# Optimization experiments

Measured on AMD Instinct MI355X. Metric: run time of the kernel, lower is better.

Reference implementation:

```python
import jax, jax.numpy as jnp
import numpy as np

N, H, V, MAX_STEPS = 256, 128, 64, 4

def setup_inputs() -> dict:
    key = jax.random.key(0)
    ks = jax.random.split(key, 16)
    def w(k, shape, fan_in):
        return jax.random.normal(k, shape, dtype=jnp.float32) / np.sqrt(fan_in)
    inp = {}
    inp['node_embeddings'] = jax.random.normal(ks[0], (N, H), dtype=jnp.float32)
    inp['skip_embeddings'] = jax.random.normal(ks[1], (N, N, H), dtype=jnp.float32)
    inp['Wx'] = w(ks[2], (H, 4 * H), H)
    inp['Wh'] = w(ks[3], (H, 4 * H), H)
    inp['b'] = jnp.zeros((4 * H,), jnp.float32)
    inp['Wxs'] = w(ks[4], (H, 4 * H), H)
    inp['Whs'] = w(ks[5], (H, 4 * H), H)
    inp['bs'] = jnp.zeros((4 * H,), jnp.float32)
    inp['Wb'] = w(ks[6], (2 * H, 2), 2 * H)
    inp['bb'] = jnp.zeros((2,), jnp.float32)
    inp['Wk'] = w(ks[7], (H, H), H)
    inp['bk'] = jnp.zeros((H,), jnp.float32)
    inp['Wq'] = w(ks[8], (2 * H, H), 2 * H)
    inp['bq'] = jnp.zeros((H,), jnp.float32)
    inp['Wl'] = w(ks[9], (2 * H, 1), 2 * H)
    inp['bl'] = jnp.zeros((1,), jnp.float32)
    inp['Wd'] = w(ks[10], (2 * H, V), 2 * H)
    inp['bd'] = jnp.zeros((V,), jnp.float32)
    # valid skips only forward in the program (include diagonal = no-skip)
    inp['skip_mask'] = jnp.triu(jnp.ones((N, N), dtype=bool))
    inp['true_indexes'] = jax.random.randint(ks[11], (N,), 0, N, dtype=jnp.int32)
    inp['false_indexes'] = jax.random.randint(ks[12], (N,), 0, N, dtype=jnp.int32)
    inp['exit_index'] = N - 1
    return inp

def _lstm(c, h, x, Wx, Wh, b):
    gates = x @ Wx + h @ Wh + b  # [..., 4H]
    i, f, g, o = jnp.split(gates, 4, axis=-1)
    c2 = jax.nn.sigmoid(f) * c + jax.nn.sigmoid(i) * jnp.tanh(g)
    h2 = jax.nn.sigmoid(o) * jnp.tanh(c2)
    return c2, h2

def reference(node_embeddings, skip_embeddings, Wx, Wh, b, Wxs, Whs, bs,
              Wb, bb, Wk, bk, Wq, bq, Wl, bl, Wd, bd,
              skip_mask, true_indexes, false_indexes, exit_index):
    n, hdim = node_embeddings.shape
    eye = jnp.eye(n, dtype=node_embeddings.dtype)
    ip0 = jnp.zeros((n,), node_embeddings.dtype).at[0].set(1.0)
    c0 = jnp.zeros((n, hdim), node_embeddings.dtype)
    h0 = jnp.zeros((n, hdim), node_embeddings.dtype)
    keys = skip_embeddings @ Wk + bk  # [N,N,H] (input-only, precompute)

    def step(carry, _):
        ip, c, h = carry
        # per-node LSTM proposals
        c_p, h_p = _lstm(c, h, node_embeddings, Wx, Wh, b)  # [N,H]
        hid = jnp.concatenate([c_p, h_p], axis=-1)  # [N,2H]
        # skip proposals: carry of source i applied to skip embedding (i,j)
        c_sk, h_sk = _lstm(c[:, None, :], h[:, None, :], skip_embeddings, Wxs, Whs, bs)  # [N,N,H]
        # branch decisions
        branch = jax.nn.softmax(hid @ Wb + bb, axis=-1)  # [N,2]
        # skip decisions (per source i, softmax over destinations j)
        queries = hid @ Wq + bq  # [N,H]
        kq = jax.nn.relu(jnp.concatenate(
            [keys, jnp.broadcast_to(queries[:, None, :], (n, n, hdim))], axis=-1))  # [N,N,2H]
        logits = jnp.einsum('ijk,kl->ijl', kq, Wl)[..., 0] + bl[0]  # [N,N]
        skip_dec = jax.nn.softmax(jnp.where(skip_mask, logits, -jnp.inf), axis=-1)
        # aggregation (IPA)
        yes_skip = skip_dec * (1.0 - eye)  # zero diagonal
        no_skip = jnp.diagonal(skip_dec)
        p_bt = ip * no_skip * branch[:, 0]
        p_bf = ip * no_skip * branch[:, 1]
        new_ip = (jax.ops.segment_sum(p_bt, true_indexes, num_segments=n)
                  + jax.ops.segment_sum(p_bf, false_indexes, num_segments=n)
                  + jnp.einsum('i,ij->j', ip, yes_skip))
        denom = new_ip[:, None] + 1e-7
        def agg(hp, hsk):
            t = jax.ops.segment_sum(hp * p_bt[:, None], true_indexes, num_segments=n)
            f = jax.ops.segment_sum(hp * p_bf[:, None], false_indexes, num_segments=n)
            s = jnp.einsum('ijh,i,ij->jh', hsk, ip, yes_skip)
            return (t + f + s) / denom
        return (new_ip, agg(c_p, c_sk), agg(h_p, h_sk)), None

    (ip, c, h), _ = jax.lax.scan(step, (ip0, c0, h0), None, length=MAX_STEPS)
    exit_concat = jnp.concatenate([c[exit_index], h[exit_index]], axis=-1)  # [2H]
    return exit_concat @ Wd + bd  # [V]
```

## Files before the change

kernel.cpp:

```cpp
#include <hip/hip_runtime.h>
#include <hip/hip_bf16.h>

constexpr int NN = 256;
constexpr int HH = 128;
constexpr int GG = 512;
constexpr int NP = NN * NN;

typedef __attribute__((ext_vector_type(8))) short short8;
typedef __attribute__((ext_vector_type(4))) float f32x4;

__device__ unsigned short g_xs[(size_t)NP * GG];
__device__ unsigned short g_wfr[20 * 512 * 8];
__device__ float g_bsp[GG];
__device__ float g_pwh[HH * HH * 4];
__device__ float g_pws[HH * HH * 4];
__device__ float g_kterm[NP];
__device__ float g_yesw[NP];
__device__ float g_noskip[NN];
__device__ float g_xg[NN * GG];
__device__ float g_hws[NN * HH * 4];
__device__ float g_c[NN * HH];
__device__ float g_h[NN * HH];
__device__ float g_sc[NN * HH];
__device__ float g_sh[NN * HH];
__device__ float g_ip[NN];
__device__ float g_nip[NN];

__device__ __forceinline__ unsigned short f2bf(float f) {
  unsigned int u = __float_as_uint(f);
  u = (u + 0x7fffu + ((u >> 16) & 1u)) >> 16;
  return (unsigned short)u;
}
__device__ __forceinline__ float bf2f(unsigned short s) {
  return __uint_as_float(((unsigned int)s) << 16);
}
__device__ __forceinline__ float frcp(float x) {
#if __has_builtin(__builtin_amdgcn_rcpf)
  return __builtin_amdgcn_rcpf(x);
#else
  return 1.0f / x;
#endif
}
__device__ __forceinline__ float sigm(float x) { return frcp(1.f + __expf(-x)); }
__device__ __forceinline__ float tanhfast(float x) { return 1.f - 2.f * frcp(__expf(2.f * x) + 1.f); }

__global__ void k_init() {
  int idx = blockIdx.x * blockDim.x + threadIdx.x;
  g_sc[idx] = 0.f; g_sh[idx] = 0.f; g_c[idx] = 0.f; g_h[idx] = 0.f;
  *(float4*)&g_hws[(size_t)idx * 4] = make_float4(0.f, 0.f, 0.f, 0.f);
  if (idx < NN) { g_nip[idx] = 0.f; g_ip[idx] = (idx == 0) ? 1.f : 0.f; }
}

__global__ __launch_bounds__(512) void k_prep(const float* __restrict__ Wxs,
                                              const float* __restrict__ Wk,
                                              const float* __restrict__ bs) {
  const int bidx = blockIdx.x;
  const int tile = bidx >> 2, ks = bidx & 3;
  const int s = threadIdx.x;
  const int ct = s >> 6, l = s & 63;
  const int c = ct * 16 + (l & 15);
  const int kbase = ks * 32 + (l >> 4) * 8;
  int src = 0;
  if (tile < 4) src = (c & 3) * 128 + tile * 32 + (c >> 2);
  unsigned short* dst = &g_wfr[((size_t)bidx * 512 + s) * 8];
#pragma unroll
  for (int e = 0; e < 8; ++e) {
    int k = kbase + e;
    float v = (tile < 4) ? Wxs[k * GG + src] : Wk[k * HH + c];
    dst[e] = f2bf(v);
  }
  if (tile < 4 && ks == 0 && (l >> 4) == 0) g_bsp[tile * 128 + c] = bs[src];
}

__global__ __launch_bounds__(128) void k_prep2(const float* __restrict__ Wh,
                                               const float* __restrict__ Whs) {
  const int k = blockIdx.x, t = threadIdx.x;
  float4 a = make_float4(Wh[k * GG + t], Wh[k * GG + 128 + t], Wh[k * GG + 256 + t], Wh[k * GG + 384 + t]);
  float4 s = make_float4(Whs[k * GG + t], Whs[k * GG + 128 + t], Whs[k * GG + 256 + t], Whs[k * GG + 384 + t]);
  *(float4*)&g_pwh[((size_t)k * HH + t) * 4] = a;
  *(float4*)&g_pws[((size_t)k * HH + t) * 4] = s;
}

__global__ __launch_bounds__(128) void k_xg(const float* __restrict__ NE,
                                            const float* __restrict__ Wx,
                                            const float* __restrict__ b) {
  const int i = blockIdx.x, t = threadIdx.x;
  __shared__ float ne[HH];
  ne[t] = NE[i * HH + t];
  __syncthreads();
  float a0 = b[t], a1 = b[128 + t], a2 = b[256 + t], a3 = b[384 + t];
  for (int k = 0; k < HH; ++k) {
    float x = ne[k];
    a0 = fmaf(x, Wx[k * GG + t], a0);
    a1 = fmaf(x, Wx[k * GG + 128 + t], a1);
    a2 = fmaf(x, Wx[k * GG + 256 + t], a2);
    a3 = fmaf(x, Wx[k * GG + 384 + t], a3);
  }
  g_xg[i * GG + t] = a0; g_xg[i * GG + 128 + t] = a1;
  g_xg[i * GG + 256 + t] = a2; g_xg[i * GG + 384 + t] = a3;
}

__device__ __forceinline__ void loadB(short8* dst, int tile, int ks, int l) {
  const unsigned short* wf = &g_wfr[((size_t)(tile * 4 + ks)) * 4096 + l * 8];
#pragma unroll
  for (int ct = 0; ct < 8; ++ct) dst[ct] = *(const short8*)(wf + ct * 512);
}

__global__ __launch_bounds__(256) void k_gemm(const float* __restrict__ SE,
                                              const float* __restrict__ bk,
                                              const float* __restrict__ Wl) {
  __shared__ __align__(16) char lds[32768];
  const int bid = blockIdx.x;
  const int pb = (bid < 128) ? (bid * 2) : ((bid - 128) * 2 + 1);
  const int pairBase = pb * 128;
  const int tid = threadIdx.x;

  for (int cc = tid; cc < 2048; cc += 256) {
    int row = cc >> 4, kc = cc & 15;
    const float* src = SE + (size_t)(pairBase + row) * HH + kc * 8;
    float4 f0 = *(const float4*)(src);
    float4 f1 = *(const float4*)(src + 4);
    short8 v;
    v[0] = (short)f2bf(f0.x); v[1] = (short)f2bf(f0.y); v[2] = (short)f2bf(f0.z); v[3] = (short)f2bf(f0.w);
    v[4] = (short)f2bf(f1.x); v[5] = (short)f2bf(f1.y); v[6] = (short)f2bf(f1.z); v[7] = (short)f2bf(f1.w);
    *(short8*)(lds + row * 256 + ((kc * 16) ^ ((row & 7) << 4))) = v;
  }
  __syncthreads();

  const int wv = tid >> 6;
  const int l = tid & 63;
  const int l15 = l & 15, lg = l >> 4;

#pragma unroll 1
  for (int tile = 0; tile < 5; ++tile) {
    f32x4 acc[2][8];
#pragma unroll
    for (int rt = 0; rt < 2; ++rt)
#pragma unroll
      for (int ct = 0; ct < 8; ++ct) acc[rt][ct] = (f32x4){0.f, 0.f, 0.f, 0.f};

    short8 bA[8], bB[8];
    loadB(bA, tile, 0, l);
#pragma unroll
    for (int ks = 0; ks < 4; ks += 2) {
      loadB(bB, tile, ks + 1, l);
      {
        const int kb = ks * 64 + lg * 16;
        short8 a[2];
#pragma unroll
        for (int rt = 0; rt < 2; ++rt) {
          int row = wv * 32 + rt * 16 + l15;
          a[rt] = *(const short8*)(lds + row * 256 + (kb ^ ((row & 7) << 4)));
        }
#pragma unroll
        for (int rt = 0; rt < 2; ++rt)
#pragma unroll
          for (int ct = 0; ct < 8; ++ct)
            acc[rt][ct] = __builtin_amdgcn_mfma_f32_16x16x32_bf16(a[rt], bA[ct], acc[rt][ct], 0, 0, 0);
      }
      if (ks + 2 < 4) loadB(bA, tile, ks + 2, l);
      {
        const int kb = (ks + 1) * 64 + lg * 16;
        short8 a[2];
#pragma unroll
        for (int rt = 0; rt < 2; ++rt) {
          int row = wv * 32 + rt * 16 + l15;
          a[rt] = *(const short8*)(lds + row * 256 + (kb ^ ((row & 7) << 4)));
        }
#pragma unroll
        for (int rt = 0; rt < 2; ++rt)
#pragma unroll
          for (int ct = 0; ct < 8; ++ct)
            acc[rt][ct] = __builtin_amdgcn_mfma_f32_16x16x32_bf16(a[rt], bB[ct], acc[rt][ct], 0, 0, 0);
      }
    }

    if (tile < 4) {
#pragma unroll
      for (int rt = 0; rt < 2; ++rt)
#pragma unroll
        for (int ct = 0; ct < 8; ++ct) {
          const int col = ct * 16 + l15;
          const float bsv = g_bsp[tile * 128 + col];
#pragma unroll
          for (int r = 0; r < 4; ++r) {
            int row = wv * 32 + rt * 16 + lg * 4 + r;
            int pair = pairBase + row;
            int jj = pair & 255, ii = pair >> 8;
            if (jj > ii) g_xs[(size_t)pair * GG + tile * 128 + col] = f2bf(acc[rt][ct][r] + bsv);
          }
        }
    } else {
#pragma unroll
      for (int rt = 0; rt < 2; ++rt) {
#pragma unroll
        for (int r = 0; r < 4; ++r) {
          float s = 0.f;
#pragma unroll
          for (int ct = 0; ct < 8; ++ct) {
            int col = ct * 16 + l15;
            float x = acc[rt][ct][r] + bk[col];
            x = fmaxf(x, 0.f);
            s = fmaf(x, Wl[col], s);
          }
#pragma unroll
          for (int m = 1; m < 16; m <<= 1) s += __shfl_xor(s, m, 64);
          int row = wv * 32 + rt * 16 + lg * 4 + r;
          int pair = pairBase + row;
          int jj = pair & 255, ii = pair >> 8;
          if (l15 == 0 && jj >= ii) g_kterm[pair] = s;
        }
      }
    }
  }
}

__global__ __launch_bounds__(256) void k_softmax() {
  const int i = blockIdx.x, j = threadIdx.x;
  __shared__ float sm[NN];
  float x = -1e30f;
  if (j >= i) x = g_kterm[i * NN + j];
  sm[j] = x;
  __syncthreads();
  for (int s = 128; s > 0; s >>= 1) { if (j < s) sm[j] = fmaxf(sm[j], sm[j + s]); __syncthreads(); }
  float mx = sm[0];
  __syncthreads();
  float e = (j >= i) ? __expf(x - mx) : 0.f;
  sm[j] = e;
  __syncthreads();
  for (int s = 128; s > 0; s >>= 1) { if (j < s) sm[j] += sm[j + s]; __syncthreads(); }
  float p = e * frcp(sm[0]);
  g_yesw[i * NN + j] = (j == i) ? 0.f : p;
  if (j == i) g_noskip[i] = p;
}

__global__ __launch_bounds__(128) void k_step(const float* __restrict__ Wb,
                                              const float* __restrict__ bb,
                                              const int* __restrict__ tix,
                                              const int* __restrict__ fix) {
  const int t = threadIdx.x;
  if (blockIdx.x < 256) {
    const int i = blockIdx.x;
    __shared__ float hsm[HH];
    __shared__ float red[2][2];
    hsm[t] = g_h[i * HH + t];
    __syncthreads();
    float a0 = g_xg[i * GG + t], a1 = g_xg[i * GG + 128 + t];
    float a2 = g_xg[i * GG + 256 + t], a3 = g_xg[i * GG + 384 + t];
    for (int k = 0; k < HH; ++k) {
      float hv = hsm[k];
      const float4 wa = *(const float4*)&g_pwh[((size_t)k * HH + t) * 4];
      a0 = fmaf(hv, wa.x, a0); a1 = fmaf(hv, wa.y, a1);
      a2 = fmaf(hv, wa.z, a2); a3 = fmaf(hv, wa.w, a3);
    }
    float co = g_c[i * HH + t];
    float c2 = sigm(a1) * co + sigm(a0) * tanhfast(a2);
    float h2 = sigm(a3) * tanhfast(c2);
    float q0 = c2 * Wb[2 * t] + h2 * Wb[2 * (128 + t)];
    float q1 = c2 * Wb[2 * t + 1] + h2 * Wb[2 * (128 + t) + 1];
#pragma unroll
    for (int m = 1; m < 64; m <<= 1) { q0 += __shfl_xor(q0, m, 64); q1 += __shfl_xor(q1, m, 64); }
    if ((t & 63) == 0) { red[t >> 6][0] = q0; red[t >> 6][1] = q1; }
    __syncthreads();
    float l0 = red[0][0] + red[1][0] + bb[0];
    float l1 = red[0][1] + red[1][1] + bb[1];
    float mm = fmaxf(l0, l1);
    float e0 = __expf(l0 - mm), e1 = __expf(l1 - mm);
    float inv = frcp(e0 + e1);
    float ipv = g_ip[i] * g_noskip[i];
    if (ipv != 0.f) {
      float pbt = ipv * e0 * inv, pbf = ipv * e1 * inv;
      int ti = tix[i], fi = fix[i];
      atomicAdd(&g_sc[ti * HH + t], c2 * pbt);
      atomicAdd(&g_sh[ti * HH + t], h2 * pbt);
      atomicAdd(&g_sc[fi * HH + t], c2 * pbf);
      atomicAdd(&g_sh[fi * HH + t], h2 * pbf);
      if (t == 0) { atomicAdd(&g_nip[ti], pbt); atomicAdd(&g_nip[fi], pbf); }
    }
  } else {
    const int idx = blockIdx.x - 256;
    const int j = idx >> 4, chunk = idx & 15;
    const int i0 = chunk * 16;
    if (i0 >= j) return;
    const int iN = (j - i0 < 16) ? (j - i0) : 16;
    __shared__ float wsh[16];
    if (t < 16) wsh[t] = (t < iN) ? g_ip[i0 + t] * g_yesw[(i0 + t) * NN + j] : 0.f;
    __syncthreads();
    float accC = 0.f, accH = 0.f, accW = 0.f;
    for (int ii = 0; ii < iN; ++ii) {
      float wgt = wsh[ii];
      if (wgt == 0.f) continue;
      const int i = i0 + ii;
      const ushort4 gv = *(const ushort4*)&g_xs[((size_t)(i * NN + j) * 128 + t) * 4];
      float4 hw = *(const float4*)&g_hws[((size_t)i * HH + t) * 4];
      float xi = bf2f(gv.x) + hw.x;
      float xf = bf2f(gv.y) + hw.y;
      float xg = bf2f(gv.z) + hw.z;
      float xo = bf2f(gv.w) + hw.w;
      float c2 = sigm(xf) * g_c[i * HH + t] + sigm(xi) * tanhfast(xg);
      float h2 = sigm(xo) * tanhfast(c2);
      accC = fmaf(wgt, c2, accC);
      accH = fmaf(wgt, h2, accH);
      accW += wgt;
    }
    if (accW != 0.f) {
      atomicAdd(&g_sc[j * HH + t], accC);
      atomicAdd(&g_sh[j * HH + t], accH);
      if (t == 0) atomicAdd(&g_nip[j], accW);
    }
  }
}

__global__ __launch_bounds__(256) void k_finish(const int last) {
  const int j = blockIdx.x, tid = threadIdx.x;
  const int t = tid & 127, half = tid >> 7;
  __shared__ float hsm[HH];
  __shared__ float4 part[2][HH];
  if (half == 0) {
    float nip = g_nip[j];
    float d = frcp(nip + 1e-7f);
    float cv = g_sc[j * HH + t] * d;
    float hv = g_sh[j * HH + t] * d;
    g_c[j * HH + t] = cv;
    g_h[j * HH + t] = hv;
    hsm[t] = hv;
    g_sc[j * HH + t] = 0.f;
    g_sh[j * HH + t] = 0.f;
    if (t == 0) { g_ip[j] = nip; g_nip[j] = 0.f; }
  }
  __syncthreads();
  if (last) return;
  float s0 = 0.f, s1 = 0.f, s2 = 0.f, s3 = 0.f;
  const int k0 = half * 64;
  for (int k = k0; k < k0 + 64; ++k) {
    float hk = hsm[k];
    const float4 w = *(const float4*)&g_pws[((size_t)k * HH + t) * 4];
    s0 = fmaf(hk, w.x, s0); s1 = fmaf(hk, w.y, s1);
    s2 = fmaf(hk, w.z, s2); s3 = fmaf(hk, w.w, s3);
  }
  part[half][t] = make_float4(s0, s1, s2, s3);
  __syncthreads();
  if (half == 0) {
    float4 a = part[0][t], bq = part[1][t];
    *(float4*)&g_hws[((size_t)j * HH + t) * 4] =
        make_float4(a.x + bq.x, a.y + bq.y, a.z + bq.z, a.w + bq.w);
  }
}

__global__ __launch_bounds__(64) void k_out(const float* __restrict__ Wd,
                                            const float* __restrict__ bd,
                                            const int* __restrict__ ei,
                                            float* __restrict__ out) {
  const int v = threadIdx.x;
  const int e = ei[0];
  float s = bd[v];
  for (int h = 0; h < HH; ++h) {
    s = fmaf(g_c[e * HH + h], Wd[h * 64 + v], s);
    s = fmaf(g_h[e * HH + h], Wd[(128 + h) * 64 + v], s);
  }
  out[v] = s;
}

extern "C" void kernel_launch(void* const* d_in, const int* in_sizes, int n_in,
                              void* d_out, int out_size, void* d_ws, size_t ws_size,
                              hipStream_t stream) {
  const float* NE  = (const float*)d_in[0];
  const float* SE  = (const float*)d_in[1];
  const float* Wx  = (const float*)d_in[2];
  const float* Wh  = (const float*)d_in[3];
  const float* b   = (const float*)d_in[4];
  const float* Wxs = (const float*)d_in[5];
  const float* Whs = (const float*)d_in[6];
  const float* bs  = (const float*)d_in[7];
  const float* Wb  = (const float*)d_in[8];
  const float* bb  = (const float*)d_in[9];
  const float* Wk  = (const float*)d_in[10];
  const float* bk  = (const float*)d_in[11];
  const float* Wl  = (const float*)d_in[14];
  const float* Wd  = (const float*)d_in[16];
  const float* bd  = (const float*)d_in[17];
  const int* tix = (const int*)d_in[19];
  const int* fix = (const int*)d_in[20];
  const int* ei  = (const int*)d_in[21];
  float* out = (float*)d_out;

  k_init<<<256, 128, 0, stream>>>();
  k_prep<<<20, 512, 0, stream>>>(Wxs, Wk, bs);
  k_prep2<<<128, 128, 0, stream>>>(Wh, Whs);
  k_xg<<<256, 128, 0, stream>>>(NE, Wx, b);
  k_gemm<<<384, 256, 0, stream>>>(SE, bk, Wl);
  k_softmax<<<256, 256, 0, stream>>>();
  for (int s = 0; s < 4; ++s) {
    k_step<<<256 + 4096, 128, 0, stream>>>(Wb, bb, tix, fix);
    k_finish<<<256, 256, 0, stream>>>(s == 3);
  }
  k_out<<<1, 64, 0, stream>>>(Wd, bd, ei, out);
}
```

Measured before the change: 165.7 us.

## Split gemm tiles across grid and move Wh gate matvec into finish kernel

The projection GEMM now gives each of its five output tiles its own block through a 2D grid instead of looping over them inside one block. That raises parallelism, but every block re-stages the same bf16-converted A rows into LDS, so the global reads and conversions happen five times. The h@Wh recurrent matvec moves from k_step into k_finish, which now runs 512 threads and computes both the Wh and Whs products, storing the full non-skip gate preactivations in g_xga. This shortens the per-node path in k_step at the cost of a larger finish kernel and one extra buffer.

```diff
diff --git a/kernel.cpp b/kernel.cpp
--- a/kernel.cpp
+++ b/kernel.cpp
@@ -17,7 +17,8 @@
 __device__ float g_kterm[NP];
 __device__ float g_yesw[NP];
 __device__ float g_noskip[NN];
-__device__ float g_xg[NN * GG];
+__device__ float g_xg[NN * HH * 4];
+__device__ float g_xga[NN * HH * 4];
 __device__ float g_hws[NN * HH * 4];
 __device__ float g_c[NN * HH];
 __device__ float g_h[NN * HH];
@@ -96,8 +97,9 @@
     a2 = fmaf(x, Wx[k * GG + 256 + t], a2);
     a3 = fmaf(x, Wx[k * GG + 384 + t], a3);
   }
-  g_xg[i * GG + t] = a0; g_xg[i * GG + 128 + t] = a1;
-  g_xg[i * GG + 256 + t] = a2; g_xg[i * GG + 384 + t] = a3;
+  float4 v = make_float4(a0, a1, a2, a3);
+  *(float4*)&g_xg[((size_t)i * HH + t) * 4] = v;
+  *(float4*)&g_xga[((size_t)i * HH + t) * 4] = v;
 }
 
 __device__ __forceinline__ void loadB(short8* dst, int tile, int ks, int l) {
@@ -111,6 +113,7 @@
                                               const float* __restrict__ Wl) {
   __shared__ __align__(16) char lds[32768];
   const int bid = blockIdx.x;
+  const int tile = blockIdx.y;
   const int pb = (bid < 128) ? (bid * 2) : ((bid - 128) * 2 + 1);
   const int pairBase = pb * 128;
   const int tid = threadIdx.x;
@@ -131,85 +134,82 @@
   const int l = tid & 63;
   const int l15 = l & 15, lg = l >> 4;
 
-#pragma unroll 1
-  for (int tile = 0; tile < 5; ++tile) {
-    f32x4 acc[2][8];
+  f32x4 acc[2][8];
+#pragma unroll
+  for (int rt = 0; rt < 2; ++rt)
+#pragma unroll
+    for (int ct = 0; ct < 8; ++ct) acc[rt][ct] = (f32x4){0.f, 0.f, 0.f, 0.f};
+
+  short8 bA[8], bB[8];
+  loadB(bA, tile, 0, l);
+#pragma unroll
+  for (int ks = 0; ks < 4; ks += 2) {
+    loadB(bB, tile, ks + 1, l);
+    {
+      const int kb = ks * 64 + lg * 16;
+      short8 a[2];
+#pragma unroll
+      for (int rt = 0; rt < 2; ++rt) {
+        int row = wv * 32 + rt * 16 + l15;
+        a[rt] = *(const short8*)(lds + row * 256 + (kb ^ ((row & 7) << 4)));
+      }
+#pragma unroll
+      for (int rt = 0; rt < 2; ++rt)
+#pragma unroll
+        for (int ct = 0; ct < 8; ++ct)
+          acc[rt][ct] = __builtin_amdgcn_mfma_f32_16x16x32_bf16(a[rt], bA[ct], acc[rt][ct], 0, 0, 0);
+    }
+    if (ks + 2 < 4) loadB(bA, tile, ks + 2, l);
+    {
+      const int kb = (ks + 1) * 64 + lg * 16;
+      short8 a[2];
+#pragma unroll
+      for (int rt = 0; rt < 2; ++rt) {
+        int row = wv * 32 + rt * 16 + l15;
+        a[rt] = *(const short8*)(lds + row * 256 + (kb ^ ((row & 7) << 4)));
+      }
+#pragma unroll
+      for (int rt = 0; rt < 2; ++rt)
+#pragma unroll
+        for (int ct = 0; ct < 8; ++ct)
+          acc[rt][ct] = __builtin_amdgcn_mfma_f32_16x16x32_bf16(a[rt], bB[ct], acc[rt][ct], 0, 0, 0);
+    }
+  }
+
+  if (tile < 4) {
 #pragma unroll
     for (int rt = 0; rt < 2; ++rt)
 #pragma unroll
-      for (int ct = 0; ct < 8; ++ct) acc[rt][ct] = (f32x4){0.f, 0.f, 0.f, 0.f};
-
-    short8 bA[8], bB[8];
-    loadB(bA, tile, 0, l);
-#pragma unroll
-    for (int ks = 0; ks < 4; ks += 2) {
-      loadB(bB, tile, ks + 1, l);
-      {
-        const int kb = ks * 64 + lg * 16;
-        short8 a[2];
-#pragma unroll
-        for (int rt = 0; rt < 2; ++rt) {
-          int row = wv * 32 + rt * 16 + l15;
-          a[rt] = *(const short8*)(lds + row * 256 + (kb ^ ((row & 7) << 4)));
-        }
-#pragma unroll
-        for (int rt = 0; rt < 2; ++rt)
-#pragma unroll
-          for (int ct = 0; ct < 8; ++ct)
-            acc[rt][ct] = __builtin_amdgcn_mfma_f32_16x16x32_bf16(a[rt], bA[ct], acc[rt][ct], 0, 0, 0);
-      }
-      if (ks + 2 < 4) loadB(bA, tile, ks + 2, l);
-      {
-        const int kb = (ks + 1) * 64 + lg * 16;
-        short8 a[2];
-#pragma unroll
-        for (int rt = 0; rt < 2; ++rt) {
-          int row = wv * 32 + rt * 16 + l15;
-          a[rt] = *(const short8*)(lds + row * 256 + (kb ^ ((row & 7) << 4)));
-        }
-#pragma unroll
-        for (int rt = 0; rt < 2; ++rt)
-#pragma unroll
-          for (int ct = 0; ct < 8; ++ct)
-            acc[rt][ct] = __builtin_amdgcn_mfma_f32_16x16x32_bf16(a[rt], bB[ct], acc[rt][ct], 0, 0, 0);
-      }
-    }
-
-    if (tile < 4) {
-#pragma unroll
-      for (int rt = 0; rt < 2; ++rt)
-#pragma unroll
-        for (int ct = 0; ct < 8; ++ct) {
-          const int col = ct * 16 + l15;
-          const float bsv = g_bsp[tile * 128 + col];
-#pragma unroll
-          for (int r = 0; r < 4; ++r) {
-            int row = wv * 32 + rt * 16 + lg * 4 + r;
-            int pair = pairBase + row;
-            int jj = pair & 255, ii = pair >> 8;
-            if (jj > ii) g_xs[(size_t)pair * GG + tile * 128 + col] = f2bf(acc[rt][ct][r] + bsv);
-          }
-        }
-    } else {
-#pragma unroll
-      for (int rt = 0; rt < 2; ++rt) {
+      for (int ct = 0; ct < 8; ++ct) {
+        const int col = ct * 16 + l15;
+        const float bsv = g_bsp[tile * 128 + col];
 #pragma unroll
         for (int r = 0; r < 4; ++r) {
-          float s = 0.f;
-#pragma unroll
-          for (int ct = 0; ct < 8; ++ct) {
-            int col = ct * 16 + l15;
-            float x = acc[rt][ct][r] + bk[col];
-            x = fmaxf(x, 0.f);
-            s = fmaf(x, Wl[col], s);
-          }
-#pragma unroll
-          for (int m = 1; m < 16; m <<= 1) s += __shfl_xor(s, m, 64);
           int row = wv * 32 + rt * 16 + lg * 4 + r;
           int pair = pairBase + row;
           int jj = pair & 255, ii = pair >> 8;
-          if (l15 == 0 && jj >= ii) g_kterm[pair] = s;
+          if (jj > ii) g_xs[(size_t)pair * GG + tile * 128 + col] = f2bf(acc[rt][ct][r] + bsv);
         }
+      }
+  } else {
+#pragma unroll
+    for (int rt = 0; rt < 2; ++rt) {
+#pragma unroll
+      for (int r = 0; r < 4; ++r) {
+        float s = 0.f;
+#pragma unroll
+        for (int ct = 0; ct < 8; ++ct) {
+          int col = ct * 16 + l15;
+          float x = acc[rt][ct][r] + bk[col];
+          x = fmaxf(x, 0.f);
+          s = fmaf(x, Wl[col], s);
+        }
+#pragma unroll
+        for (int m = 1; m < 16; m <<= 1) s += __shfl_xor(s, m, 64);
+        int row = wv * 32 + rt * 16 + lg * 4 + r;
+        int pair = pairBase + row;
+        int jj = pair & 255, ii = pair >> 8;
+        if (l15 == 0 && jj >= ii) g_kterm[pair] = s;
       }
     }
   }
@@ -241,21 +241,11 @@
   const int t = threadIdx.x;
   if (blockIdx.x < 256) {
     const int i = blockIdx.x;
-    __shared__ float hsm[HH];
     __shared__ float red[2][2];
-    hsm[t] = g_h[i * HH + t];
-    __syncthreads();
-    float a0 = g_xg[i * GG + t], a1 = g_xg[i * GG + 128 + t];
-    float a2 = g_xg[i * GG + 256 + t], a3 = g_xg[i * GG + 384 + t];
-    for (int k = 0; k < HH; ++k) {
-      float hv = hsm[k];
-      const float4 wa = *(const float4*)&g_pwh[((size_t)k * HH + t) * 4];
-      a0 = fmaf(hv, wa.x, a0); a1 = fmaf(hv, wa.y, a1);
-      a2 = fmaf(hv, wa.z, a2); a3 = fmaf(hv, wa.w, a3);
-    }
+    const float4 a = *(const float4*)&g_xga[((size_t)i * HH + t) * 4];
     float co = g_c[i * HH + t];
-    float c2 = sigm(a1) * co + sigm(a0) * tanhfast(a2);
-    float h2 = sigm(a3) * tanhfast(c2);
+    float c2 = sigm(a.y) * co + sigm(a.x) * tanhfast(a.z);
+    float h2 = sigm(a.w) * tanhfast(c2);
     float q0 = c2 * Wb[2 * t] + h2 * Wb[2 * (128 + t)];
     float q1 = c2 * Wb[2 * t + 1] + h2 * Wb[2 * (128 + t) + 1];
 #pragma unroll
@@ -311,12 +301,12 @@
   }
 }
 
-__global__ __launch_bounds__(256) void k_finish(const int last) {
+__global__ __launch_bounds__(512) void k_finish(const int last) {
   const int j = blockIdx.x, tid = threadIdx.x;
-  const int t = tid & 127, half = tid >> 7;
+  const int t = tid & 127, sel = tid >> 7;
   __shared__ float hsm[HH];
-  __shared__ float4 part[2][HH];
-  if (half == 0) {
+  __shared__ float4 part[4][HH];
+  if (sel == 0) {
     float nip = g_nip[j];
     float d = frcp(nip + 1e-7f);
     float cv = g_sc[j * HH + t] * d;
@@ -330,20 +320,28 @@
   }
   __syncthreads();
   if (last) return;
+  const float* __restrict__ W = (sel >> 1) ? g_pws : g_pwh;
+  const int k0 = (sel & 1) * 64;
   float s0 = 0.f, s1 = 0.f, s2 = 0.f, s3 = 0.f;
-  const int k0 = half * 64;
+#pragma unroll 8
   for (int k = k0; k < k0 + 64; ++k) {
     float hk = hsm[k];
-    const float4 w = *(const float4*)&g_pws[((size_t)k * HH + t) * 4];
+    const float4 w = *(const float4*)&W[((size_t)k * HH + t) * 4];
     s0 = fmaf(hk, w.x, s0); s1 = fmaf(hk, w.y, s1);
     s2 = fmaf(hk, w.z, s2); s3 = fmaf(hk, w.w, s3);
   }
-  part[half][t] = make_float4(s0, s1, s2, s3);
-  __syncthreads();
-  if (half == 0) {
-    float4 a = part[0][t], bq = part[1][t];
+  part[sel][t] = make_float4(s0, s1, s2, s3);
+  __syncthreads();
+  if (sel == 0) {
+    float4 p0 = part[0][t], p1 = part[1][t];
+    float4 xg = *(const float4*)&g_xg[((size_t)j * HH + t) * 4];
+    *(float4*)&g_xga[((size_t)j * HH + t) * 4] =
+        make_float4(xg.x + p0.x + p1.x, xg.y + p0.y + p1.y,
+                    xg.z + p0.z + p1.z, xg.w + p0.w + p1.w);
+  } else if (sel == 2) {
+    float4 p2 = part[2][t], p3 = part[3][t];
     *(float4*)&g_hws[((size_t)j * HH + t) * 4] =
-        make_float4(a.x + bq.x, a.y + bq.y, a.z + bq.z, a.w + bq.w);
+        make_float4(p2.x + p3.x, p2.y + p3.y, p2.z + p3.z, p2.w + p3.w);
   }
 }
 
@@ -388,11 +386,11 @@
   k_prep<<<20, 512, 0, stream>>>(Wxs, Wk, bs);
   k_prep2<<<128, 128, 0, stream>>>(Wh, Whs);
   k_xg<<<256, 128, 0, stream>>>(NE, Wx, b);
-  k_gemm<<<384, 256, 0, stream>>>(SE, bk, Wl);
+  k_gemm<<<dim3(384, 5), 256, 0, stream>>>(SE, bk, Wl);
   k_softmax<<<256, 256, 0, stream>>>();
   for (int s = 0; s < 4; ++s) {
     k_step<<<256 + 4096, 128, 0, stream>>>(Wb, bb, tix, fix);
-    k_finish<<<256, 256, 0, stream>>>(s == 3);
+    k_finish<<<256, 512, 0, stream>>>(s == 3);
   }
   k_out<<<1, 64, 0, stream>>>(Wd, bd, ei, out);
 }
```

Result: faster. 156.4 us (-5.6%).
